# Kernel optimization log

Measured on AMD Instinct MI355X. Metric: run time of the kernel, lower is better.

Reference implementation:

```python
import jax, jax.numpy as jnp
import numpy as np
import math

B, S, D_MODEL, D_K = 4, 4096, 1024, 256

def setup_inputs() -> dict:
    key = jax.random.key(0)
    ks = jax.random.split(key, 9)
    def xavier(k, shape):
        fan_out, fan_in = shape
        limit = math.sqrt(6.0 / (fan_in + fan_out))
        return jax.random.uniform(k, shape, jnp.float32, -limit, limit)
    return {
        "_q": jax.random.normal(ks[0], (B, S, D_MODEL), jnp.float32),
        "_k": jax.random.normal(ks[1], (B, S, D_MODEL), jnp.float32),
        "_v": jax.random.normal(ks[2], (B, S, D_MODEL), jnp.float32),
        "mask": jnp.ones((B, 1, S), dtype=bool),  # unused by the original forward
        "Wq": xavier(ks[3], (D_K, D_MODEL)),
        "bq": jnp.zeros((D_K,), jnp.float32),
        "Wk": xavier(ks[4], (D_K, D_MODEL)),
        "bk": jnp.zeros((D_K,), jnp.float32),
        "Wv": xavier(ks[5], (D_K, D_MODEL)),
        "bv": jnp.zeros((D_K,), jnp.float32),
    }

def reference(_q, _k, _v, mask, Wq, bq, Wk, bk, Wv, bv):
    # Linear projections: x @ W.T + b  (torch nn.Linear semantics)
    q = jnp.einsum('bsm,km->bsk', _q, Wq) + bq  # [B,S,d_k]
    k = jnp.einsum('bsm,km->bsk', _k, Wk) + bk
    v = jnp.einsum('bsm,km->bsk', _v, Wv) + bv
    scores = jnp.einsum('bqk,bsk->bqs', q, k) / math.sqrt(D_K)  # [B,S,S]
    atten = jax.nn.softmax(scores, axis=-1)
    out = jnp.einsum('bqs,bsk->bqk', atten, v)  # [B,S,d_k]
    return out
```

## Files before the change

kernel.cpp:

```cpp
#include <hip/hip_runtime.h>
#include <stdint.h>

#define DEV static __device__ __forceinline__

typedef __bf16 bf16x8 __attribute__((ext_vector_type(8)));
typedef float f32x4 __attribute__((ext_vector_type(4)));

typedef const __attribute__((address_space(1))) void* as1cp;
typedef __attribute__((address_space(3))) void* as3p;

DEV uint32_t f2bf1(float f) {
  uint32_t u = __builtin_bit_cast(uint32_t, f);
  u += 0x7fffu + ((u >> 16) & 1u);
  return u >> 16;
}
DEV uint32_t f2bf2(float lo, float hi) { return f2bf1(lo) | (f2bf1(hi) << 16); }

DEV void gll16(const void* g, void* l) {
  __builtin_amdgcn_global_load_lds((as1cp)g, (as3p)l, 16, 0, 0);
}

__global__ __launch_bounds__(512) void proj_kernel(
    const float* __restrict__ xq, const float* __restrict__ xk, const float* __restrict__ xv,
    const float* __restrict__ wq, const float* __restrict__ wk, const float* __restrict__ wv,
    const float* __restrict__ bq, const float* __restrict__ bk, const float* __restrict__ bv,
    uint16_t* __restrict__ qo, uint16_t* __restrict__ ko, uint16_t* __restrict__ vo)
{
  const int z = blockIdx.z;
  const float* X  = (z == 0) ? xq : (z == 1) ? xk : xv;
  const float* W  = (z == 0) ? wq : (z == 1) ? wk : wv;
  const float* Bi = (z == 0) ? bq : (z == 1) ? bk : bv;

  const int tid = threadIdx.x;
  const int lane = tid & 63;
  const int w = tid >> 6;
  const int wm = w >> 2, wn = w & 3;
  const int l15 = lane & 15, g = lane >> 4;
  const int m0 = blockIdx.x * 128;

  __shared__ uint16_t sA[128 * 64];
  __shared__ uint16_t sB[256 * 64];

  const int am = tid >> 2, ak = (tid & 3) * 16;
  const int bn = tid >> 1, bkc = (tid & 1) * 32;

  const float* Ap = X + (size_t)(m0 + am) * 1024 + ak;
  const float* Wp = W + (size_t)bn * 1024 + bkc;

  f32x4 acc[4][4];
  #pragma unroll
  for (int i = 0; i < 4; ++i)
    #pragma unroll
    for (int j = 0; j < 4; ++j) { f32x4 zz = {0.f, 0.f, 0.f, 0.f}; acc[i][j] = zz; }

  float ar[16], br[32];
  #pragma unroll
  for (int i = 0; i < 4; ++i) { float4 t = ((const float4*)Ap)[i];
    ar[4*i+0]=t.x; ar[4*i+1]=t.y; ar[4*i+2]=t.z; ar[4*i+3]=t.w; }
  #pragma unroll
  for (int i = 0; i < 8; ++i) { float4 t = ((const float4*)Wp)[i];
    br[4*i+0]=t.x; br[4*i+1]=t.y; br[4*i+2]=t.z; br[4*i+3]=t.w; }

  for (int kt = 0; kt < 16; ++kt) {
    if (kt) __syncthreads();
    {
      uint32_t ph = (uint32_t)(am * 128 + ak * 2) ^ ((uint32_t)(am & 7) << 4);
      uint4 p0, p1;
      p0.x = f2bf2(ar[0],  ar[1]);  p0.y = f2bf2(ar[2],  ar[3]);
      p0.z = f2bf2(ar[4],  ar[5]);  p0.w = f2bf2(ar[6],  ar[7]);
      p1.x = f2bf2(ar[8],  ar[9]);  p1.y = f2bf2(ar[10], ar[11]);
      p1.z = f2bf2(ar[12], ar[13]); p1.w = f2bf2(ar[14], ar[15]);
      *(uint4*)((char*)sA + ph)        = p0;
      *(uint4*)((char*)sA + (ph ^ 16)) = p1;
      uint32_t pb = (uint32_t)(bn * 128 + bkc * 2) ^ ((uint32_t)(bn & 7) << 4);
      #pragma unroll
      for (int c = 0; c < 4; ++c) {
        uint4 pq;
        pq.x = f2bf2(br[8*c+0], br[8*c+1]); pq.y = f2bf2(br[8*c+2], br[8*c+3]);
        pq.z = f2bf2(br[8*c+4], br[8*c+5]); pq.w = f2bf2(br[8*c+6], br[8*c+7]);
        *(uint4*)((char*)sB + (pb ^ (16 * c))) = pq;
      }
    }
    __syncthreads();
    if (kt < 15) {
      const float* Ap2 = Ap + (kt + 1) * 64;
      const float* Wp2 = Wp + (kt + 1) * 64;
      #pragma unroll
      for (int i = 0; i < 4; ++i) { float4 t = ((const float4*)Ap2)[i];
        ar[4*i+0]=t.x; ar[4*i+1]=t.y; ar[4*i+2]=t.z; ar[4*i+3]=t.w; }
      #pragma unroll
      for (int i = 0; i < 8; ++i) { float4 t = ((const float4*)Wp2)[i];
        br[4*i+0]=t.x; br[4*i+1]=t.y; br[4*i+2]=t.z; br[4*i+3]=t.w; }
    }
    #pragma unroll
    for (int ks = 0; ks < 2; ++ks) {
      bf16x8 fa[4], fb[4];
      #pragma unroll
      for (int f = 0; f < 4; ++f) {
        uint32_t row = wm * 64 + 16 * f + l15;
        fa[f] = *(const bf16x8*)((char*)sA + row * 128 +
                 (((uint32_t)(ks * 64 + g * 16)) ^ ((row & 7) << 4)));
      }
      #pragma unroll
      for (int f = 0; f < 4; ++f) {
        uint32_t row = wn * 64 + 16 * f + l15;
        fb[f] = *(const bf16x8*)((char*)sB + row * 128 +
                 (((uint32_t)(ks * 64 + g * 16)) ^ ((row & 7) << 4)));
      }
      #pragma unroll
      for (int fm = 0; fm < 4; ++fm)
        #pragma unroll
        for (int fn = 0; fn < 4; ++fn)
          acc[fm][fn] = __builtin_amdgcn_mfma_f32_16x16x32_bf16(fa[fm], fb[fn], acc[fm][fn], 0, 0, 0);
    }
  }

  #pragma unroll
  for (int fn = 0; fn < 4; ++fn) {
    const int n = wn * 64 + 16 * fn + l15;
    const float bias = Bi[n];
    #pragma unroll
    for (int fm = 0; fm < 4; ++fm) {
      const int mg = m0 + wm * 64 + 16 * fm + 4 * g;
      if (z == 0) {
        #pragma unroll
        for (int r = 0; r < 4; ++r)
          qo[(size_t)(mg + r) * 256 + n] =
              (uint16_t)f2bf1((acc[fm][fn][r] + bias) * 0.09016844f);
      } else if (z == 1) {
        #pragma unroll
        for (int r = 0; r < 4; ++r)
          ko[(size_t)(mg + r) * 256 + n] = (uint16_t)f2bf1(acc[fm][fn][r] + bias);
      } else {
        uint2 pv;
        pv.x = f2bf2(acc[fm][fn][0] + bias, acc[fm][fn][1] + bias);
        pv.y = f2bf2(acc[fm][fn][2] + bias, acc[fm][fn][3] + bias);
        *(uint2*)(vo + (((size_t)(mg >> 12)) << 20) + (((size_t)n) << 12) + (mg & 4095)) = pv;
      }
    }
  }
}

__global__ __launch_bounds__(256) void attn_kernel(
    const uint16_t* __restrict__ qg, const uint16_t* __restrict__ kg,
    const uint16_t* __restrict__ vg, float* __restrict__ out)
{
  extern __shared__ char smem[];
  char* sKb = smem;
  char* sVb = smem + 65536;
  char* sPb = smem + 131072;

  const int bid = blockIdx.x;
  const int xcd = bid & 7, slot = bid >> 3;
  const int batch = xcd >> 1;
  const int q0 = ((((xcd & 1) << 5) + slot)) * 64;

  const int tid = threadIdx.x;
  const int lane = tid & 63;
  const int w = tid >> 6;
  const int l15 = lane & 15, g = lane >> 4;
  const int wbase = tid & ~63;

  const size_t rowb = (size_t)batch * 4096;

  bf16x8 qf[8];
  {
    const uint16_t* qp = qg + (rowb + q0 + w * 16 + l15) * 256;
    #pragma unroll
    for (int ks = 0; ks < 8; ++ks) qf[ks] = *(const bf16x8*)(qp + ks * 32 + g * 8);
  }

  f32x4 o[16];
  #pragma unroll
  for (int i = 0; i < 16; ++i) { f32x4 zz = {0.f, 0.f, 0.f, 0.f}; o[i] = zz; }
  float mrow[4], lrow[4];
  #pragma unroll
  for (int r = 0; r < 4; ++r) { mrow[r] = -1e30f; lrow[r] = 0.f; }

  const char* kgb = (const char*)(kg + rowb * 256);
  const char* vgb = (const char*)(vg + (size_t)batch * 256 * 4096);

  auto STAGE = [&](int buf, int t) {
    const int kv0 = t * 64;
    #pragma unroll
    for (int i = 0; i < 8; ++i) {
      const int widx = i * 256 + wbase;
      uint32_t L = (uint32_t)(widx + lane) * 16;
      uint32_t U = L ^ (((L >> 9) & 7u) << 4);
      const char* src = kgb + (size_t)(kv0 + (U >> 9)) * 512 + (U & 511);
      gll16(src, sKb + buf * 32768 + widx * 16);
    }
    #pragma unroll
    for (int i = 0; i < 8; ++i) {
      const int widx = i * 256 + wbase;
      uint32_t L = (uint32_t)(widx + lane) * 16;
      uint32_t U = L ^ (((L >> 7) & 7u) << 4);
      const char* src = vgb + (size_t)(U >> 7) * 8192 + (size_t)kv0 * 2 + (U & 127);
      gll16(src, sVb + buf * 32768 + widx * 16);
    }
  };

  STAGE(0, 0);
  char* Pw = sPb + w * 2048;

  for (int t = 0; t < 64; ++t) {
    __syncthreads();
    if (t + 1 < 64) STAGE((t + 1) & 1, t + 1);

    const char* Kb = sKb + (t & 1) * 32768;
    const char* Vb = sVb + (t & 1) * 32768;

    f32x4 s4[4];
    #pragma unroll
    for (int f = 0; f < 4; ++f) { f32x4 zz = {0.f, 0.f, 0.f, 0.f}; s4[f] = zz; }
    #pragma unroll
    for (int ks = 0; ks < 8; ++ks) {
      bf16x8 kf[4];
      #pragma unroll
      for (int f = 0; f < 4; ++f) {
        uint32_t row = 16 * f + l15;
        kf[f] = *(const bf16x8*)(Kb + row * 512 +
                 (((uint32_t)(ks * 64 + g * 16)) ^ ((row & 7) << 4)));
      }
      #pragma unroll
      for (int f = 0; f < 4; ++f)
        s4[f] = __builtin_amdgcn_mfma_f32_16x16x32_bf16(qf[ks], kf[f], s4[f], 0, 0, 0);
    }

    float sc[4], ps[4][4];
    #pragma unroll
    for (int r = 0; r < 4; ++r) {
      float mx = fmaxf(fmaxf(s4[0][r], s4[1][r]), fmaxf(s4[2][r], s4[3][r]));
      mx = fmaxf(mx, __shfl_xor(mx, 1, 64));
      mx = fmaxf(mx, __shfl_xor(mx, 2, 64));
      mx = fmaxf(mx, __shfl_xor(mx, 4, 64));
      mx = fmaxf(mx, __shfl_xor(mx, 8, 64));
      float mn = fmaxf(mrow[r], mx);
      sc[r] = exp2f(mrow[r] - mn);
      mrow[r] = mn;
      float sum = 0.f;
      #pragma unroll
      for (int f = 0; f < 4; ++f) { ps[f][r] = exp2f(s4[f][r] - mn); sum += ps[f][r]; }
      sum += __shfl_xor(sum, 1, 64);
      sum += __shfl_xor(sum, 2, 64);
      sum += __shfl_xor(sum, 4, 64);
      sum += __shfl_xor(sum, 8, 64);
      lrow[r] = lrow[r] * sc[r] + sum;
    }
    #pragma unroll
    for (int i = 0; i < 16; ++i)
      #pragma unroll
      for (int r = 0; r < 4; ++r) o[i][r] *= sc[r];

    #pragma unroll
    for (int f = 0; f < 4; ++f)
      #pragma unroll
      for (int r = 0; r < 4; ++r) {
        uint32_t row = 4 * g + r;
        *(uint16_t*)(Pw + row * 128 +
            (((uint32_t)((16 * f + l15) * 2)) ^ ((row & 7) << 4))) = (uint16_t)f2bf1(ps[f][r]);
      }

    #pragma unroll
    for (int ks2 = 0; ks2 < 2; ++ks2) {
      bf16x8 pa = *(const bf16x8*)(Pw + l15 * 128 +
                   (((uint32_t)(ks2 * 64 + g * 16)) ^ ((l15 & 7) << 4)));
      #pragma unroll
      for (int fd = 0; fd < 16; ++fd) {
        uint32_t row = 16 * fd + l15;
        bf16x8 vb = *(const bf16x8*)(Vb + row * 128 +
                     (((uint32_t)(ks2 * 64 + g * 16)) ^ ((row & 7) << 4)));
        o[fd] = __builtin_amdgcn_mfma_f32_16x16x32_bf16(pa, vb, o[fd], 0, 0, 0);
      }
    }
  }

  float* op = out + (rowb + q0 + w * 16) * 256;
  #pragma unroll
  for (int r = 0; r < 4; ++r) {
    float inv = 1.f / lrow[r];
    #pragma unroll
    for (int fd = 0; fd < 16; ++fd)
      op[(4 * g + r) * 256 + 16 * fd + l15] = o[fd][r] * inv;
  }
}

extern "C" void kernel_launch(void* const* d_in, const int* in_sizes, int n_in,
                              void* d_out, int out_size, void* d_ws, size_t ws_size,
                              hipStream_t stream) {
  const float* xq = (const float*)d_in[0];
  const float* xk = (const float*)d_in[1];
  const float* xv = (const float*)d_in[2];
  const float* wq = (const float*)d_in[4];
  const float* bq = (const float*)d_in[5];
  const float* wk = (const float*)d_in[6];
  const float* bk = (const float*)d_in[7];
  const float* wv = (const float*)d_in[8];
  const float* bv = (const float*)d_in[9];

  uint16_t* qws = (uint16_t*)d_ws;
  uint16_t* kws = qws + (size_t)4 * 4096 * 256;
  uint16_t* vws = kws + (size_t)4 * 4096 * 256;

  proj_kernel<<<dim3(128, 1, 3), 512, 0, stream>>>(
      xq, xk, xv, wq, wk, wv, bq, bk, bv, qws, kws, vws);

  (void)hipFuncSetAttribute((const void*)attn_kernel,
                            hipFuncAttributeMaxDynamicSharedMemorySize, 139264);
  attn_kernel<<<dim3(256), 256, 139264, stream>>>(qws, kws, vws, (float*)d_out);
}
```

Before: 513.0 us.

## Split KV across wave halves in attention, retile projection, add lazy rescale

The attention kernel doubles its block to 512 threads and splits each KV tile between two wave groups, each processing 32 keys. The two partial softmax states are merged at the end through shared memory, with the second half's output staged as bf16. It also skips the output rescale unless the running max grows by more than a threshold, and re-lays out V staging. The projection kernel moves to 128x128 tiles over a 2D grid of 256-thread blocks with occupancy hints. The aim is more waves in flight and fewer rescale multiplies, at the cost of a merge step and an extra bf16 rounding of half the partial output.

```diff
diff --git a/kernel.cpp b/kernel.cpp
--- a/kernel.cpp
+++ b/kernel.cpp
@@ -15,12 +15,13 @@
   return u >> 16;
 }
 DEV uint32_t f2bf2(float lo, float hi) { return f2bf1(lo) | (f2bf1(hi) << 16); }
+DEV float bf2f(uint32_t h) { return __builtin_bit_cast(float, h << 16); }
 
 DEV void gll16(const void* g, void* l) {
   __builtin_amdgcn_global_load_lds((as1cp)g, (as3p)l, 16, 0, 0);
 }
 
-__global__ __launch_bounds__(512) void proj_kernel(
+__global__ __launch_bounds__(256, 3) void proj_kernel(
     const float* __restrict__ xq, const float* __restrict__ xk, const float* __restrict__ xv,
     const float* __restrict__ wq, const float* __restrict__ wk, const float* __restrict__ wv,
     const float* __restrict__ bq, const float* __restrict__ bk, const float* __restrict__ bv,
@@ -34,18 +35,17 @@
   const int tid = threadIdx.x;
   const int lane = tid & 63;
   const int w = tid >> 6;
-  const int wm = w >> 2, wn = w & 3;
+  const int wm = w >> 1, wn = w & 1;
   const int l15 = lane & 15, g = lane >> 4;
   const int m0 = blockIdx.x * 128;
+  const int n0 = blockIdx.y * 128;
 
   __shared__ uint16_t sA[128 * 64];
-  __shared__ uint16_t sB[256 * 64];
-
-  const int am = tid >> 2, ak = (tid & 3) * 16;
-  const int bn = tid >> 1, bkc = (tid & 1) * 32;
-
+  __shared__ uint16_t sB[128 * 64];
+
+  const int am = tid >> 1, ak = (tid & 1) * 32;
   const float* Ap = X + (size_t)(m0 + am) * 1024 + ak;
-  const float* Wp = W + (size_t)bn * 1024 + bkc;
+  const float* Wp = W + (size_t)(n0 + am) * 1024 + ak;
 
   f32x4 acc[4][4];
   #pragma unroll
@@ -53,44 +53,42 @@
     #pragma unroll
     for (int j = 0; j < 4; ++j) { f32x4 zz = {0.f, 0.f, 0.f, 0.f}; acc[i][j] = zz; }
 
-  float ar[16], br[32];
-  #pragma unroll
-  for (int i = 0; i < 4; ++i) { float4 t = ((const float4*)Ap)[i];
+  float ar[32];
+  #pragma unroll
+  for (int i = 0; i < 8; ++i) { float4 t = ((const float4*)Ap)[i];
     ar[4*i+0]=t.x; ar[4*i+1]=t.y; ar[4*i+2]=t.z; ar[4*i+3]=t.w; }
-  #pragma unroll
-  for (int i = 0; i < 8; ++i) { float4 t = ((const float4*)Wp)[i];
-    br[4*i+0]=t.x; br[4*i+1]=t.y; br[4*i+2]=t.z; br[4*i+3]=t.w; }
+
+  const uint32_t ph = (uint32_t)(am * 128 + ak * 2) ^ ((uint32_t)(am & 7) << 4);
 
   for (int kt = 0; kt < 16; ++kt) {
     if (kt) __syncthreads();
+    #pragma unroll
+    for (int c = 0; c < 4; ++c) {
+      uint4 p;
+      p.x = f2bf2(ar[8*c+0], ar[8*c+1]); p.y = f2bf2(ar[8*c+2], ar[8*c+3]);
+      p.z = f2bf2(ar[8*c+4], ar[8*c+5]); p.w = f2bf2(ar[8*c+6], ar[8*c+7]);
+      *(uint4*)((char*)sA + (ph ^ (16u * c))) = p;
+    }
     {
-      uint32_t ph = (uint32_t)(am * 128 + ak * 2) ^ ((uint32_t)(am & 7) << 4);
-      uint4 p0, p1;
-      p0.x = f2bf2(ar[0],  ar[1]);  p0.y = f2bf2(ar[2],  ar[3]);
-      p0.z = f2bf2(ar[4],  ar[5]);  p0.w = f2bf2(ar[6],  ar[7]);
-      p1.x = f2bf2(ar[8],  ar[9]);  p1.y = f2bf2(ar[10], ar[11]);
-      p1.z = f2bf2(ar[12], ar[13]); p1.w = f2bf2(ar[14], ar[15]);
-      *(uint4*)((char*)sA + ph)        = p0;
-      *(uint4*)((char*)sA + (ph ^ 16)) = p1;
-      uint32_t pb = (uint32_t)(bn * 128 + bkc * 2) ^ ((uint32_t)(bn & 7) << 4);
+      float wr[32];
+      const float* Wk = Wp + kt * 64;
+      #pragma unroll
+      for (int i = 0; i < 8; ++i) { float4 t = ((const float4*)Wk)[i];
+        wr[4*i+0]=t.x; wr[4*i+1]=t.y; wr[4*i+2]=t.z; wr[4*i+3]=t.w; }
       #pragma unroll
       for (int c = 0; c < 4; ++c) {
-        uint4 pq;
-        pq.x = f2bf2(br[8*c+0], br[8*c+1]); pq.y = f2bf2(br[8*c+2], br[8*c+3]);
-        pq.z = f2bf2(br[8*c+4], br[8*c+5]); pq.w = f2bf2(br[8*c+6], br[8*c+7]);
-        *(uint4*)((char*)sB + (pb ^ (16 * c))) = pq;
+        uint4 p;
+        p.x = f2bf2(wr[8*c+0], wr[8*c+1]); p.y = f2bf2(wr[8*c+2], wr[8*c+3]);
+        p.z = f2bf2(wr[8*c+4], wr[8*c+5]); p.w = f2bf2(wr[8*c+6], wr[8*c+7]);
+        *(uint4*)((char*)sB + (ph ^ (16u * c))) = p;
       }
     }
     __syncthreads();
     if (kt < 15) {
       const float* Ap2 = Ap + (kt + 1) * 64;
-      const float* Wp2 = Wp + (kt + 1) * 64;
-      #pragma unroll
-      for (int i = 0; i < 4; ++i) { float4 t = ((const float4*)Ap2)[i];
+      #pragma unroll
+      for (int i = 0; i < 8; ++i) { float4 t = ((const float4*)Ap2)[i];
         ar[4*i+0]=t.x; ar[4*i+1]=t.y; ar[4*i+2]=t.z; ar[4*i+3]=t.w; }
-      #pragma unroll
-      for (int i = 0; i < 8; ++i) { float4 t = ((const float4*)Wp2)[i];
-        br[4*i+0]=t.x; br[4*i+1]=t.y; br[4*i+2]=t.z; br[4*i+3]=t.w; }
     }
     #pragma unroll
     for (int ks = 0; ks < 2; ++ks) {
@@ -117,7 +115,7 @@
 
   #pragma unroll
   for (int fn = 0; fn < 4; ++fn) {
-    const int n = wn * 64 + 16 * fn + l15;
+    const int n = n0 + wn * 64 + 16 * fn + l15;
     const float bias = Bi[n];
     #pragma unroll
     for (int fm = 0; fm < 4; ++fm) {
@@ -141,31 +139,28 @@
   }
 }
 
-__global__ __launch_bounds__(256) void attn_kernel(
+__global__ __launch_bounds__(512) void attn_kernel(
     const uint16_t* __restrict__ qg, const uint16_t* __restrict__ kg,
     const uint16_t* __restrict__ vg, float* __restrict__ out)
 {
   extern __shared__ char smem[];
-  char* sKb = smem;
-  char* sVb = smem + 65536;
-  char* sPb = smem + 131072;
 
   const int bid = blockIdx.x;
   const int xcd = bid & 7, slot = bid >> 3;
   const int batch = xcd >> 1;
-  const int q0 = ((((xcd & 1) << 5) + slot)) * 64;
+  const int q0 = (((xcd & 1) << 5) + slot) * 64;
 
   const int tid = threadIdx.x;
   const int lane = tid & 63;
   const int w = tid >> 6;
+  const int hv = w >> 2;
+  const int wq = w & 3;
   const int l15 = lane & 15, g = lane >> 4;
-  const int wbase = tid & ~63;
-
   const size_t rowb = (size_t)batch * 4096;
 
   bf16x8 qf[8];
   {
-    const uint16_t* qp = qg + (rowb + q0 + w * 16 + l15) * 256;
+    const uint16_t* qp = qg + (rowb + q0 + wq * 16 + l15) * 256;
     #pragma unroll
     for (int ks = 0; ks < 8; ++ks) qf[ks] = *(const bf16x8*)(qp + ks * 32 + g * 8);
   }
@@ -180,108 +175,146 @@
   const char* kgb = (const char*)(kg + rowb * 256);
   const char* vgb = (const char*)(vg + (size_t)batch * 256 * 4096);
 
-  auto STAGE = [&](int buf, int t) {
-    const int kv0 = t * 64;
-    #pragma unroll
-    for (int i = 0; i < 8; ++i) {
-      const int widx = i * 256 + wbase;
-      uint32_t L = (uint32_t)(widx + lane) * 16;
+  auto STAGE = [&](int h, int buf, int t) {
+    const int kv0 = (2 * t + h) * 32;
+    char* kd = smem + (size_t)(h * 2 + buf) * 16384;
+    char* vd = smem + 65536 + (size_t)(h * 2 + buf) * 16384;
+    #pragma unroll
+    for (int r2 = 0; r2 < 2; ++r2) {
+      uint32_t L = (uint32_t)(tid + r2 * 512) * 16;
       uint32_t U = L ^ (((L >> 9) & 7u) << 4);
-      const char* src = kgb + (size_t)(kv0 + (U >> 9)) * 512 + (U & 511);
-      gll16(src, sKb + buf * 32768 + widx * 16);
-    }
-    #pragma unroll
-    for (int i = 0; i < 8; ++i) {
-      const int widx = i * 256 + wbase;
-      uint32_t L = (uint32_t)(widx + lane) * 16;
-      uint32_t U = L ^ (((L >> 7) & 7u) << 4);
-      const char* src = vgb + (size_t)(U >> 7) * 8192 + (size_t)kv0 * 2 + (U & 127);
-      gll16(src, sVb + buf * 32768 + widx * 16);
+      gll16(kgb + (size_t)(kv0 + (U >> 9)) * 512 + (U & 511), kd + L);
+      uint32_t d = L >> 6;
+      uint32_t kvo = (L >> 4) & 3u;
+      gll16(vgb + (size_t)d * 8192 + (size_t)(kv0 + 8 * kvo) * 2, vd + L);
     }
   };
 
-  STAGE(0, 0);
-  char* Pw = sPb + w * 2048;
+  STAGE(0, 0, 0); STAGE(1, 0, 0);
+  char* Pw = smem + 131072 + (size_t)w * 1024;
+  int buf = 0;
 
   for (int t = 0; t < 64; ++t) {
     __syncthreads();
-    if (t + 1 < 64) STAGE((t + 1) & 1, t + 1);
-
-    const char* Kb = sKb + (t & 1) * 32768;
-    const char* Vb = sVb + (t & 1) * 32768;
-
-    f32x4 s4[4];
-    #pragma unroll
-    for (int f = 0; f < 4; ++f) { f32x4 zz = {0.f, 0.f, 0.f, 0.f}; s4[f] = zz; }
+    if (t + 1 < 64) { STAGE(0, buf ^ 1, t + 1); STAGE(1, buf ^ 1, t + 1); }
+
+    const char* Kb = smem + (size_t)(hv * 2 + buf) * 16384;
+    const char* Vb = smem + 65536 + (size_t)(hv * 2 + buf) * 16384;
+
+    f32x4 s4[2];
+    #pragma unroll
+    for (int f = 0; f < 2; ++f) { f32x4 zz = {0.f, 0.f, 0.f, 0.f}; s4[f] = zz; }
     #pragma unroll
     for (int ks = 0; ks < 8; ++ks) {
-      bf16x8 kf[4];
-      #pragma unroll
-      for (int f = 0; f < 4; ++f) {
+      bf16x8 kf[2];
+      #pragma unroll
+      for (int f = 0; f < 2; ++f) {
         uint32_t row = 16 * f + l15;
         kf[f] = *(const bf16x8*)(Kb + row * 512 +
-                 (((uint32_t)(ks * 64 + g * 16)) ^ ((row & 7) << 4)));
-      }
-      #pragma unroll
-      for (int f = 0; f < 4; ++f)
+                 (((uint32_t)(ks * 64 + g * 16)) ^ ((l15 & 7) << 4)));
+      }
+      #pragma unroll
+      for (int f = 0; f < 2; ++f)
         s4[f] = __builtin_amdgcn_mfma_f32_16x16x32_bf16(qf[ks], kf[f], s4[f], 0, 0, 0);
     }
 
-    float sc[4], ps[4][4];
+    float mx[4];
     #pragma unroll
     for (int r = 0; r < 4; ++r) {
-      float mx = fmaxf(fmaxf(s4[0][r], s4[1][r]), fmaxf(s4[2][r], s4[3][r]));
-      mx = fmaxf(mx, __shfl_xor(mx, 1, 64));
-      mx = fmaxf(mx, __shfl_xor(mx, 2, 64));
-      mx = fmaxf(mx, __shfl_xor(mx, 4, 64));
-      mx = fmaxf(mx, __shfl_xor(mx, 8, 64));
-      float mn = fmaxf(mrow[r], mx);
-      sc[r] = exp2f(mrow[r] - mn);
-      mrow[r] = mn;
+      float m2 = fmaxf(s4[0][r], s4[1][r]);
+      m2 = fmaxf(m2, __shfl_xor(m2, 1, 64));
+      m2 = fmaxf(m2, __shfl_xor(m2, 2, 64));
+      m2 = fmaxf(m2, __shfl_xor(m2, 4, 64));
+      m2 = fmaxf(m2, __shfl_xor(m2, 8, 64));
+      mx[r] = m2;
+    }
+    int stable = (mx[0] <= mrow[0] + 8.f) && (mx[1] <= mrow[1] + 8.f) &&
+                 (mx[2] <= mrow[2] + 8.f) && (mx[3] <= mrow[3] + 8.f);
+    if (!__all(stable)) {
+      float sc[4];
+      #pragma unroll
+      for (int r = 0; r < 4; ++r) {
+        float mn = fmaxf(mrow[r], mx[r]);
+        sc[r] = exp2f(mrow[r] - mn);
+        mrow[r] = mn;
+        lrow[r] *= sc[r];
+      }
+      #pragma unroll
+      for (int j = 0; j < 16; ++j)
+        #pragma unroll
+        for (int r = 0; r < 4; ++r) o[j][r] *= sc[r];
+    }
+    float ps[2][4];
+    #pragma unroll
+    for (int r = 0; r < 4; ++r) {
       float sum = 0.f;
       #pragma unroll
-      for (int f = 0; f < 4; ++f) { ps[f][r] = exp2f(s4[f][r] - mn); sum += ps[f][r]; }
+      for (int f = 0; f < 2; ++f) { ps[f][r] = exp2f(s4[f][r] - mrow[r]); sum += ps[f][r]; }
       sum += __shfl_xor(sum, 1, 64);
       sum += __shfl_xor(sum, 2, 64);
       sum += __shfl_xor(sum, 4, 64);
       sum += __shfl_xor(sum, 8, 64);
-      lrow[r] = lrow[r] * sc[r] + sum;
-    }
-    #pragma unroll
-    for (int i = 0; i < 16; ++i)
-      #pragma unroll
-      for (int r = 0; r < 4; ++r) o[i][r] *= sc[r];
-
-    #pragma unroll
-    for (int f = 0; f < 4; ++f)
-      #pragma unroll
-      for (int r = 0; r < 4; ++r) {
-        uint32_t row = 4 * g + r;
-        *(uint16_t*)(Pw + row * 128 +
-            (((uint32_t)((16 * f + l15) * 2)) ^ ((row & 7) << 4))) = (uint16_t)f2bf1(ps[f][r]);
-      }
-
-    #pragma unroll
-    for (int ks2 = 0; ks2 < 2; ++ks2) {
-      bf16x8 pa = *(const bf16x8*)(Pw + l15 * 128 +
-                   (((uint32_t)(ks2 * 64 + g * 16)) ^ ((l15 & 7) << 4)));
-      #pragma unroll
-      for (int fd = 0; fd < 16; ++fd) {
-        uint32_t row = 16 * fd + l15;
-        bf16x8 vb = *(const bf16x8*)(Vb + row * 128 +
-                     (((uint32_t)(ks2 * 64 + g * 16)) ^ ((row & 7) << 4)));
-        o[fd] = __builtin_amdgcn_mfma_f32_16x16x32_bf16(pa, vb, o[fd], 0, 0, 0);
-      }
-    }
-  }
-
-  float* op = out + (rowb + q0 + w * 16) * 256;
-  #pragma unroll
-  for (int r = 0; r < 4; ++r) {
-    float inv = 1.f / lrow[r];
+      lrow[r] += sum;
+    }
+
+    #pragma unroll
+    for (int f = 0; f < 2; ++f)
+      #pragma unroll
+      for (int r = 0; r < 4; ++r)
+        *(uint16_t*)(Pw + (4 * g + r) * 64 +
+            (((uint32_t)(32 * f + 2 * l15)) ^ ((uint32_t)g << 4))) = (uint16_t)f2bf1(ps[f][r]);
+
+    bf16x8 pa = *(const bf16x8*)(Pw + l15 * 64 + 16 * (g ^ (l15 >> 2)));
+    #pragma unroll
+    for (int fd = 0; fd < 16; ++fd) {
+      bf16x8 vbf = *(const bf16x8*)(Vb + fd * 1024 + l15 * 64 + g * 16);
+      o[fd] = __builtin_amdgcn_mfma_f32_16x16x32_bf16(pa, vbf, o[fd], 0, 0, 0);
+    }
+
+    buf ^= 1;
+  }
+
+  float*    mlb = (float*)smem;
+  uint32_t* ob  = (uint32_t*)(smem + 8192);
+  __syncthreads();
+  if (hv == 1) {
+    #pragma unroll
+    for (int r = 0; r < 4; ++r) {
+      mlb[((0 * 4 + wq) * 64 + lane) * 4 + r] = mrow[r];
+      mlb[((1 * 4 + wq) * 64 + lane) * 4 + r] = lrow[r];
+    }
     #pragma unroll
     for (int fd = 0; fd < 16; ++fd)
-      op[(4 * g + r) * 256 + 16 * fd + l15] = o[fd][r] * inv;
+      #pragma unroll
+      for (int p = 0; p < 2; ++p)
+        ob[(wq * 32 + fd * 2 + p) * 64 + lane] = f2bf2(o[fd][2 * p], o[fd][2 * p + 1]);
+  }
+  __syncthreads();
+  if (hv == 0) {
+    float a[4], b2[4], inv[4];
+    #pragma unroll
+    for (int r = 0; r < 4; ++r) {
+      float mu = mlb[((0 * 4 + wq) * 64 + lane) * 4 + r];
+      float lu = mlb[((1 * 4 + wq) * 64 + lane) * 4 + r];
+      float mn = fmaxf(mrow[r], mu);
+      a[r]  = exp2f(mrow[r] - mn);
+      b2[r] = exp2f(mu - mn);
+      inv[r] = 1.f / (lrow[r] * a[r] + lu * b2[r]);
+    }
+    float* op = out + (rowb + q0 + wq * 16) * 256;
+    #pragma unroll
+    for (int fd = 0; fd < 16; ++fd) {
+      #pragma unroll
+      for (int p = 0; p < 2; ++p) {
+        uint32_t u = ob[(wq * 32 + fd * 2 + p) * 64 + lane];
+        float vlo = bf2f(u & 0xffffu), vhi = bf2f(u >> 16);
+        int r0 = 2 * p, r1 = 2 * p + 1;
+        op[(4 * g + r0) * 256 + 16 * fd + l15] =
+            (o[fd][r0] * a[r0] + vlo * b2[r0]) * inv[r0];
+        op[(4 * g + r1) * 256 + 16 * fd + l15] =
+            (o[fd][r1] * a[r1] + vhi * b2[r1]) * inv[r1];
+      }
+    }
   }
 }
 
@@ -302,10 +335,10 @@
   uint16_t* kws = qws + (size_t)4 * 4096 * 256;
   uint16_t* vws = kws + (size_t)4 * 4096 * 256;
 
-  proj_kernel<<<dim3(128, 1, 3), 512, 0, stream>>>(
+  proj_kernel<<<dim3(128, 2, 3), 256, 0, stream>>>(
       xq, xk, xv, wq, wk, wv, bq, bk, bv, qws, kws, vws);
 
   (void)hipFuncSetAttribute((const void*)attn_kernel,
                             hipFuncAttributeMaxDynamicSharedMemorySize, 139264);
-  attn_kernel<<<dim3(256), 256, 139264, stream>>>(qws, kws, vws, (float*)d_out);
-}
+  attn_kernel<<<dim3(256), 512, 139264, stream>>>(qws, kws, vws, (float*)d_out);
+}
```

Result: faster. 446.6 us (-12.9%).
